# Kernel tuning notes

Measured on AMD Instinct MI355X. Metric: run time of the kernel, lower is better.

## Reference

```python
import jax, jax.numpy as jnp
import numpy as np

POOL = 7
IMG = 1024.0
NUM_CLASSES = 2
R = 1000


def crop_and_resize(feat, boxes, pool):
    # feat: [C,H,W]; boxes: [N,4] normalized (y1,x1,y2,x2); returns [N,C,pool,pool]
    C, H, W = feat.shape
    y1, x1, y2, x2 = boxes[:, 0], boxes[:, 1], boxes[:, 2], boxes[:, 3]
    t = jnp.arange(pool, dtype=feat.dtype) / (pool - 1)
    ys = (y1[:, None] + (y2 - y1)[:, None] * t[None, :]) * (H - 1)  # [N,P]
    xs = (x1[:, None] + (x2 - x1)[:, None] * t[None, :]) * (W - 1)  # [N,P]
    vy = (ys >= 0) & (ys <= H - 1)
    vx = (xs >= 0) & (xs <= W - 1)
    yf = jnp.floor(ys)
    xf = jnp.floor(xs)
    wy = (ys - yf)[None, :, :, None]  # [1,N,P,1]
    wx = (xs - xf)[None, :, None, :]  # [1,N,1,P]
    y0 = jnp.clip(yf, 0, H - 1).astype(jnp.int32)
    y1i = jnp.clip(yf + 1, 0, H - 1).astype(jnp.int32)
    x0 = jnp.clip(xf, 0, W - 1).astype(jnp.int32)
    x1i = jnp.clip(xf + 1, 0, W - 1).astype(jnp.int32)

    def g(yi, xi):  # gather -> [C,N,P,P]
        return feat[:, yi[:, :, None], xi[:, None, :]]

    val = (g(y0, x0) * (1 - wy) * (1 - wx)
           + g(y0, x1i) * (1 - wy) * wx
           + g(y1i, x0) * wy * (1 - wx)
           + g(y1i, x1i) * wy * wx)
    mask = (vy[:, :, None] & vx[:, None, :])[None]  # extrapolation value 0
    return jnp.where(mask, val, 0.0).transpose(1, 0, 2, 3)


def roi_align(feats, rois_flat):
    # rois_flat: [N,4] in pixel coords (x1,y1,x2,y2)
    x1, y1, x2, y2 = rois_flat[:, 0], rois_flat[:, 1], rois_flat[:, 2], rois_flat[:, 3]
    lvl = jnp.log2(jnp.sqrt((y2 - y1) * (x2 - x1)) / 224.0)
    lvl = jnp.clip(jnp.round(lvl) + 4, 2, 5)
    boxes = rois_flat[:, jnp.array([1, 0, 3, 2])] / IMG  # (y1,x1,y2,x2) normalized
    crops = jnp.stack([crop_and_resize(f[0], boxes, POOL) for f in feats])  # [4,N,C,P,P]
    sel = (lvl[None, :] == jnp.arange(2, 6, dtype=lvl.dtype)[:, None])       # [4,N]
    return jnp.sum(jnp.where(sel[:, :, None, None, None], crops, 0.0), axis=0)  # [N,C,P,P]


def setup_inputs() -> dict:
    key = jax.random.key(0)
    ks = jax.random.split(key, 24)
    feat2 = jax.random.normal(ks[0], (1, 256, 256, 256), jnp.float32)
    feat3 = jax.random.normal(ks[1], (1, 256, 128, 128), jnp.float32)
    feat4 = jax.random.normal(ks[2], (1, 256, 64, 64), jnp.float32)
    feat5 = jax.random.normal(ks[3], (1, 256, 32, 32), jnp.float32)
    x1 = jax.random.uniform(ks[4], (1, R), minval=0.0, maxval=900.0)
    y1 = jax.random.uniform(ks[5], (1, R), minval=0.0, maxval=900.0)
    w = jax.random.uniform(ks[6], (1, R), minval=16.0, maxval=400.0)
    h = jax.random.uniform(ks[7], (1, R), minval=16.0, maxval=400.0)
    rois = jnp.stack([x1, y1, jnp.minimum(x1 + w, 1023.0), jnp.minimum(y1 + h, 1023.0)], axis=-1)
    s = 0.02
    params = dict(
        conv_w=s * jax.random.normal(ks[8], (1024, 256, POOL, POOL), jnp.float32),
        conv_b=jnp.zeros((1024,), jnp.float32),
        bn_gamma=jnp.ones((1024,), jnp.float32),
        bn_beta=jnp.zeros((1024,), jnp.float32),
        bn_mean=jnp.zeros((1024,), jnp.float32),
        bn_var=jnp.ones((1024,), jnp.float32),
        fc1_w=s * jax.random.normal(ks[9], (1024, 1024), jnp.float32),
        fc1_b=jnp.zeros((1024,), jnp.float32),
        fc2_w=s * jax.random.normal(ks[10], (1024, 1024), jnp.float32),
        fc2_b=jnp.zeros((1024,), jnp.float32),
        cls_w=s * jax.random.normal(ks[11], (NUM_CLASSES, 1024), jnp.float32),
        cls_b=jnp.zeros((NUM_CLASSES,), jnp.float32),
        bbox_w=s * jax.random.normal(ks[12], (NUM_CLASSES * 4, 1024), jnp.float32),
        bbox_b=jnp.zeros((NUM_CLASSES * 4,), jnp.float32),
    )
    return dict(feat2=feat2, feat3=feat3, feat4=feat4, feat5=feat5, rois=rois, **params)


def reference(feat2, feat3, feat4, feat5, rois, conv_w, conv_b, bn_gamma, bn_beta,
              bn_mean, bn_var, fc1_w, fc1_b, fc2_w, fc2_b, cls_w, cls_b, bbox_w, bbox_b):
    roi_number = rois.shape[1]
    pooled = roi_align([feat2, feat3, feat4, feat5], rois.reshape(-1, 4))  # [N,256,7,7]
    # conv1 (7x7 valid on 7x7 input -> 1x1 spatial) + BN (inference stats, eps=1e-3)
    y = jnp.einsum('nchw,ochw->no', pooled, conv_w) + conv_b
    y = (y - bn_mean) / jnp.sqrt(bn_var + 1e-3) * bn_gamma + bn_beta
    h = jax.nn.relu(y @ fc1_w.T + fc1_b)
    h = jax.nn.relu(h @ fc2_w.T + fc2_b)
    logits = h @ cls_w.T + cls_b
    probs = jax.nn.softmax(logits, axis=-1)
    bbox = h @ bbox_w.T + bbox_b
    return (logits.reshape(1, roi_number, NUM_CLASSES),
            probs.reshape(1, roi_number, NUM_CLASSES),
            bbox.reshape(1, roi_number, NUM_CLASSES, 4))
```

## Files before the change

kernel.cpp:

```cpp
#include <hip/hip_runtime.h>
#include <cstdint>
#include <cstddef>

typedef __attribute__((ext_vector_type(8))) short bf16x8;
typedef __attribute__((ext_vector_type(4))) float f32x4;

#define POOLK 12544

#define TOFF2 0
#define TOFF3 16777216
#define TOFF4 20971520
#define TOFF5 22020096

__device__ __forceinline__ void gld16(const void* g, void* l) {
    __builtin_amdgcn_global_load_lds(
        (const __attribute__((address_space(1))) void*)g,
        (__attribute__((address_space(3))) void*)l, 16, 0, 0);
}
__device__ __forceinline__ unsigned short f32_to_bf16(float f) {
    union { float f; unsigned u; } x; x.f = f;
    return (unsigned short)((x.u + 0x7FFFu + ((x.u >> 16) & 1u)) >> 16);
}
__device__ __forceinline__ float bf16_to_f32(unsigned short s) {
    return __uint_as_float(((unsigned)s) << 16);
}

__global__ __launch_bounds__(256) void feat_tr_kernel(
    const float* __restrict__ f2, const float* __restrict__ f3,
    const float* __restrict__ f4, const float* __restrict__ f5,
    unsigned short* __restrict__ T)
{
    __shared__ __align__(16) unsigned short sh[128 * 256];
    int b = blockIdx.x;
    const float* src; unsigned short* dst; int P;
    if (b < 512)      { src = f2; dst = T + TOFF2; P = 65536; }
    else if (b < 640) { src = f3; dst = T + TOFF3; P = 16384; b -= 512; }
    else if (b < 672) { src = f4; dst = T + TOFF4; P = 4096;  b -= 640; }
    else              { src = f5; dst = T + TOFF5; P = 1024;  b -= 672; }
    const int p0 = b * 128;
    const int t = threadIdx.x;
    const int lane5 = t & 31;
    const int x4 = lane5 * 4;
    const int fx = (lane5 & 7) << 3;

#pragma unroll
    for (int it = 0; it < 8; ++it) {
        float4 v[4];
        int cs[4];
#pragma unroll
        for (int u = 0; u < 4; ++u) {
            cs[u] = it * 32 + u * 8 + (t >> 5);
            v[u] = *(const float4*)(src + (size_t)cs[u] * P + p0 + x4);
        }
#pragma unroll
        for (int u = 0; u < 4; ++u) {
            const int cp = cs[u] ^ fx;
            float vv[4] = {v[u].x, v[u].y, v[u].z, v[u].w};
#pragma unroll
            for (int i = 0; i < 4; ++i)
                sh[(x4 + i) * 256 + cp] = f32_to_bf16(vv[i]);
        }
    }
    __syncthreads();

    const int c0 = lane5 * 8;
#pragma unroll
    for (int oz = 0; oz < 16; ++oz) {
        const int pp = oz * 8 + (t >> 5);
        const int cr = c0 ^ (((pp >> 2) & 7) << 3);
        const bf16x8 vv = *(const bf16x8*)&sh[pp * 256 + cr];
        *(bf16x8*)(dst + (size_t)(p0 + pp) * 256 + c0) = vv;
    }
}

__global__ __launch_bounds__(256) void gather_prep_kernel(
    const unsigned short* __restrict__ T, const float* __restrict__ rois,
    unsigned short* __restrict__ pooled, int nroi,
    const float* __restrict__ conv_w, unsigned short* __restrict__ convw_bf,
    const float* __restrict__ fc1_w, unsigned short* __restrict__ fc1w_bf,
    const float* __restrict__ fc2_w, unsigned short* __restrict__ fc2w_bf)
{
    const int t = threadIdx.x;
    int b = blockIdx.x;

    if (b >= 1024) {
        b -= 1024;
        if (b < 2048) {
            __shared__ unsigned short sh[6272];
            const int o = b >> 1, half = b & 1;
            const float* srow = conv_w + (size_t)o * POOLK + half * 6272;
            for (int k = t; k < 6272; k += 256) sh[k] = f32_to_bf16(srow[k]);
            __syncthreads();
            unsigned short* drow = convw_bf + (size_t)o * POOLK + half * 128;
            for (int k = t; k < 6272; k += 256) {
                const int ij = k >> 7, cl = k & 127;
                drow[ij * 256 + cl] = sh[cl * 49 + ij];
            }
        } else {
            b -= 2048;
            const float* src = (b < 256) ? fc1_w : fc2_w;
            unsigned short* dst = (b < 256) ? fc1w_bf : fc2w_bf;
            const int base = (b & 255) * 4096 + t * 16;
#pragma unroll
            for (int u = 0; u < 4; ++u) {
                const float4 v = *(const float4*)(src + base + u * 4);
                ushort4 o4;
                o4.x = f32_to_bf16(v.x); o4.y = f32_to_bf16(v.y);
                o4.z = f32_to_bf16(v.z); o4.w = f32_to_bf16(v.w);
                *(ushort4*)(dst + base + u * 4) = o4;
            }
        }
        return;
    }

    const int n = b;
    unsigned short* orow = pooled + (size_t)n * POOLK;
    if (n >= nroi) {
        const bf16x8 z = {};
        for (int k = t * 8; k < POOLK; k += 2048) *(bf16x8*)(orow + k) = z;
        return;
    }
    __shared__ int sy0[7], sy1[7], sx0[7], sx1[7];
    __shared__ float swy[7], swx[7], svy[7], svx[7];

    const float rx1 = rois[n*4+0], ry1 = rois[n*4+1];
    const float rx2 = rois[n*4+2], ry2 = rois[n*4+3];
    int lvl = (int)rintf(log2f(sqrtf((ry2-ry1)*(rx2-rx1)) * (1.0f/224.0f))) + 4;
    lvl = lvl < 2 ? 2 : (lvl > 5 ? 5 : lvl);
    const int W = 256 >> (lvl - 2);
    const float Hm1 = (float)(W - 1);
    const unsigned short* Tl = T + (lvl == 2 ? TOFF2 : (lvl == 3 ? TOFF3 : (lvl == 4 ? TOFF4 : TOFF5)));

    if (t < 7) {
        const float tt = (float)t / 6.0f;
        const float by1 = ry1*(1.0f/1024.0f), by2 = ry2*(1.0f/1024.0f);
        const float bx1 = rx1*(1.0f/1024.0f), bx2 = rx2*(1.0f/1024.0f);
        const float ys = (by1 + (by2 - by1) * tt) * Hm1;
        const float xs = (bx1 + (bx2 - bx1) * tt) * Hm1;
        const float yf = floorf(ys), xf = floorf(xs);
        swy[t] = ys - yf;  swx[t] = xs - xf;
        sy0[t] = (int)fminf(fmaxf(yf,        0.0f), Hm1);
        sy1[t] = (int)fminf(fmaxf(yf + 1.0f, 0.0f), Hm1);
        sx0[t] = (int)fminf(fmaxf(xf,        0.0f), Hm1);
        sx1[t] = (int)fminf(fmaxf(xf + 1.0f, 0.0f), Hm1);
        svy[t] = (ys >= 0.0f && ys <= Hm1) ? 1.0f : 0.0f;
        svx[t] = (xs >= 0.0f && xs <= Hm1) ? 1.0f : 0.0f;
    }
    __syncthreads();

    const int g  = t >> 5;
    const int c0 = (t & 31) * 8;
#pragma unroll
    for (int it = 0; it < 7; ++it) {
        const int pos = it * 8 + g;
        if (pos >= 49) break;
        const int i = pos / 7, j = pos % 7;
        const int y0 = sy0[i], y1 = sy1[i], x0 = sx0[j], x1 = sx1[j];
        const float wy = swy[i], wx = swx[j];
        const float scale = svy[i] * svx[j];
        const bf16x8 v00 = *(const bf16x8*)(Tl + ((size_t)(y0*W + x0))*256 + c0);
        const bf16x8 v01 = *(const bf16x8*)(Tl + ((size_t)(y0*W + x1))*256 + c0);
        const bf16x8 v10 = *(const bf16x8*)(Tl + ((size_t)(y1*W + x0))*256 + c0);
        const bf16x8 v11 = *(const bf16x8*)(Tl + ((size_t)(y1*W + x1))*256 + c0);
        bf16x8 o;
#pragma unroll
        for (int jj = 0; jj < 8; ++jj) {
            const float f00 = bf16_to_f32((unsigned short)v00[jj]);
            const float f01 = bf16_to_f32((unsigned short)v01[jj]);
            const float f10 = bf16_to_f32((unsigned short)v10[jj]);
            const float f11 = bf16_to_f32((unsigned short)v11[jj]);
            const float top = f00 + (f01 - f00) * wx;
            const float bot = f10 + (f11 - f10) * wx;
            o[jj] = (short)f32_to_bf16((top + (bot - top) * wy) * scale);
        }
        *(bf16x8*)(orow + pos * 256 + c0) = o;
    }
}

__global__ __launch_bounds__(256) void roi_direct_kernel(
    const float* __restrict__ feat2, const float* __restrict__ feat3,
    const float* __restrict__ feat4, const float* __restrict__ feat5,
    const float* __restrict__ rois, unsigned short* __restrict__ pooled, int nroi)
{
    const int n = blockIdx.x;
    const int tid = threadIdx.x;
    unsigned short* orow = pooled + (size_t)n * POOLK;
    if (n >= nroi) {
        const bf16x8 z = {};
        for (int k = tid * 8; k < POOLK; k += 2048) *(bf16x8*)(orow + k) = z;
        return;
    }
    __shared__ int sy0[7], sy1[7], sx0[7], sx1[7];
    __shared__ float swy[7], swx[7], svy[7], svx[7];
    const float rx1 = rois[n*4+0], ry1 = rois[n*4+1];
    const float rx2 = rois[n*4+2], ry2 = rois[n*4+3];
    int lvl = (int)rintf(log2f(sqrtf((ry2-ry1)*(rx2-rx1)) * (1.0f/224.0f))) + 4;
    lvl = lvl < 2 ? 2 : (lvl > 5 ? 5 : lvl);
    const int H = 256 >> (lvl - 2);
    const float Hm1 = (float)(H - 1);
    const float* feat = lvl==2 ? feat2 : (lvl==3 ? feat3 : (lvl==4 ? feat4 : feat5));
    if (tid < 7) {
        const float t = (float)tid / 6.0f;
        const float by1 = ry1*(1.0f/1024.0f), by2 = ry2*(1.0f/1024.0f);
        const float bx1 = rx1*(1.0f/1024.0f), bx2 = rx2*(1.0f/1024.0f);
        const float ys = (by1 + (by2-by1)*t) * Hm1;
        const float xs = (bx1 + (bx2-bx1)*t) * Hm1;
        const float yf = floorf(ys), xf = floorf(xs);
        swy[tid] = ys - yf;  swx[tid] = xs - xf;
        sy0[tid] = (int)fminf(fmaxf(yf,      0.0f), Hm1);
        sy1[tid] = (int)fminf(fmaxf(yf+1.0f, 0.0f), Hm1);
        sx0[tid] = (int)fminf(fmaxf(xf,      0.0f), Hm1);
        sx1[tid] = (int)fminf(fmaxf(xf+1.0f, 0.0f), Hm1);
        svy[tid] = (ys >= 0.0f && ys <= Hm1) ? 1.0f : 0.0f;
        svx[tid] = (xs >= 0.0f && xs <= Hm1) ? 1.0f : 0.0f;
    }
    __syncthreads();
    const int HW = H * H;
    for (int e = tid; e < POOLK; e += 256) {
        const int c = e / 49, ij = e % 49, i = ij / 7, j = ij % 7;
        const float* p = feat + c * HW;
        const int y0 = sy0[i], y1 = sy1[i], x0 = sx0[j], x1 = sx1[j];
        const float wy = swy[i], wx = swx[j];
        const float v00 = p[y0*H + x0], v01 = p[y0*H + x1];
        const float v10 = p[y1*H + x0], v11 = p[y1*H + x1];
        float v = v00*(1.0f-wy)*(1.0f-wx) + v01*(1.0f-wy)*wx
                + v10*wy*(1.0f-wx)        + v11*wy*wx;
        v *= svy[i] * svx[j];
        orow[ij*256 + c] = f32_to_bf16(v);
    }
}

__global__ __launch_bounds__(256) void wprep_kernel(
    const float* __restrict__ conv_w, unsigned short* __restrict__ convw_bf,
    const float* __restrict__ fc1_w, unsigned short* __restrict__ fc1w_bf,
    const float* __restrict__ fc2_w, unsigned short* __restrict__ fc2w_bf)
{
    const int t = threadIdx.x;
    int b = blockIdx.x;
    if (b < 2048) {
        __shared__ unsigned short sh[6272];
        const int o = b >> 1, half = b & 1;
        const float* srow = conv_w + (size_t)o * POOLK + half * 6272;
        for (int k = t; k < 6272; k += 256) sh[k] = f32_to_bf16(srow[k]);
        __syncthreads();
        unsigned short* drow = convw_bf + (size_t)o * POOLK + half * 128;
        for (int k = t; k < 6272; k += 256) {
            const int ij = k >> 7, cl = k & 127;
            drow[ij * 256 + cl] = sh[cl * 49 + ij];
        }
        return;
    }
    b -= 2048;
    const float* src = (b < 256) ? fc1_w : fc2_w;
    unsigned short* dst = (b < 256) ? fc1w_bf : fc2w_bf;
    const int base = (b & 255) * 4096 + t * 16;
#pragma unroll
    for (int u = 0; u < 4; ++u) {
        const float4 v = *(const float4*)(src + base + u * 4);
        ushort4 o4;
        o4.x = f32_to_bf16(v.x); o4.y = f32_to_bf16(v.y);
        o4.z = f32_to_bf16(v.z); o4.w = f32_to_bf16(v.w);
        *(ushort4*)(dst + base + u * 4) = o4;
    }
}

__global__ __launch_bounds__(256, 2) void gemm_bt(
    const unsigned short* __restrict__ A, const unsigned short* __restrict__ B,
    float* __restrict__ Cpart, int K, int Kper, int nz)
{
    __shared__ __align__(16) unsigned short At[2][128*64];
    __shared__ __align__(16) unsigned short Bt[2][128*64];
    const int tid  = threadIdx.x;
    const int lane = tid & 63;
    const int bid  = blockIdx.x;
    const int z  = bid % nz;
    const int iq = bid / nz;
    const int bx = iq & 7, by = iq >> 3;
    const int wm = (tid >> 6) >> 1, wn = (tid >> 6) & 1;
    const size_t k0 = (size_t)z * Kper;

    const int r1 = tid >> 3;
    const int q  = tid & 7;
    const int csw = (q ^ (r1 & 7)) * 8;
    const unsigned short* Ag = A + ((size_t)(by * 128 + r1)) * K + k0 + csw;
    const unsigned short* Bg = B + ((size_t)(bx * 128 + r1)) * K + k0 + csw;
    const int nit = (Kper + 63) >> 6;

#pragma unroll
    for (int p = 0; p < 4; ++p) {
        gld16(Ag + (size_t)(32 * p) * K, &At[0][p * 2048 + tid * 8]);
        gld16(Bg + (size_t)(32 * p) * K, &Bt[0][p * 2048 + tid * 8]);
    }

    f32x4 acc[4][4] = {};
    const int fr = lane & 15;
    const int fq = lane >> 4;
    const int sA = fr & 7;

    int buf = 0;
    for (int it = 0; it < nit; ++it) {
        const int k = it << 6;
        if (it + 1 < nit) {
            const size_t ko = (size_t)(k + 64);
#pragma unroll
            for (int p = 0; p < 4; ++p) {
                gld16(Ag + (size_t)(32 * p) * K + ko, &At[buf ^ 1][p * 2048 + tid * 8]);
                gld16(Bg + (size_t)(32 * p) * K + ko, &Bt[buf ^ 1][p * 2048 + tid * 8]);
            }
            asm volatile("s_waitcnt vmcnt(8)" ::: "memory");
        } else {
            asm volatile("s_waitcnt vmcnt(0)" ::: "memory");
        }
        __builtin_amdgcn_sched_barrier(0);
        __builtin_amdgcn_s_barrier();
        __builtin_amdgcn_sched_barrier(0);

        bf16x8 a[4][2], b[4][2];
#pragma unroll
        for (int mi = 0; mi < 4; ++mi) {
            const int row = wm * 64 + mi * 16 + fr;
#pragma unroll
            for (int kk = 0; kk < 2; ++kk)
                a[mi][kk] = *(const bf16x8*)&At[buf][row * 64 + ((kk * 4 + fq) ^ sA) * 8];
        }
#pragma unroll
        for (int ni = 0; ni < 4; ++ni) {
            const int row = wn * 64 + ni * 16 + fr;
#pragma unroll
            for (int kk = 0; kk < 2; ++kk)
                b[ni][kk] = *(const bf16x8*)&Bt[buf][row * 64 + ((kk * 4 + fq) ^ sA) * 8];
        }
        __builtin_amdgcn_s_setprio(1);
#pragma unroll
        for (int mi = 0; mi < 4; ++mi)
#pragma unroll
            for (int ni = 0; ni < 4; ++ni)
                acc[mi][ni] = __builtin_amdgcn_mfma_f32_16x16x32_bf16(
                    a[mi][0], b[ni][0], acc[mi][ni], 0, 0, 0);
        if (k + 32 < Kper) {
#pragma unroll
            for (int mi = 0; mi < 4; ++mi)
#pragma unroll
                for (int ni = 0; ni < 4; ++ni)
                    acc[mi][ni] = __builtin_amdgcn_mfma_f32_16x16x32_bf16(
                        a[mi][1], b[ni][1], acc[mi][ni], 0, 0, 0);
        }
        __builtin_amdgcn_s_setprio(0);
        __builtin_amdgcn_sched_barrier(0);
        __builtin_amdgcn_s_barrier();
        __builtin_amdgcn_sched_barrier(0);
        buf ^= 1;
    }

    float* Cp = Cpart + (size_t)z * (1024 * 1024);
    const int row0 = by * 128 + wm * 64;
    const int col0 = bx * 128 + wn * 64;
#pragma unroll
    for (int mi = 0; mi < 4; ++mi)
#pragma unroll
        for (int ni = 0; ni < 4; ++ni)
#pragma unroll
            for (int r = 0; r < 4; ++r)
                Cp[(size_t)(row0 + mi*16 + fq*4 + r) * 1024 + col0 + ni*16 + fr]
                    = acc[mi][ni][r];
}

__global__ void reduce_bn_kernel(const float* __restrict__ part,
    const float* __restrict__ bias, const float* __restrict__ gamma,
    const float* __restrict__ beta, const float* __restrict__ mean,
    const float* __restrict__ var, unsigned short* __restrict__ out, int nz)
{
    const int i4 = (blockIdx.x * 256 + threadIdx.x) * 4;
    const int n = i4 & 1023;
    float4 v = make_float4(0.f, 0.f, 0.f, 0.f);
    for (int zz = 0; zz < nz; ++zz) {
        const float4 p = *(const float4*)(part + (size_t)zz * 1048576 + i4);
        v.x += p.x; v.y += p.y; v.z += p.z; v.w += p.w;
    }
    const float4 bi = *(const float4*)(bias + n);
    const float4 ga = *(const float4*)(gamma + n);
    const float4 be = *(const float4*)(beta + n);
    const float4 me = *(const float4*)(mean + n);
    const float4 va = *(const float4*)(var + n);
    ushort4 o;
    o.x = f32_to_bf16((v.x + bi.x - me.x) * __frsqrt_rn(va.x + 0.001f) * ga.x + be.x);
    o.y = f32_to_bf16((v.y + bi.y - me.y) * __frsqrt_rn(va.y + 0.001f) * ga.y + be.y);
    o.z = f32_to_bf16((v.z + bi.z - me.z) * __frsqrt_rn(va.z + 0.001f) * ga.z + be.z);
    o.w = f32_to_bf16((v.w + bi.w - me.w) * __frsqrt_rn(va.w + 0.001f) * ga.w + be.w);
    *(ushort4*)(out + i4) = o;
}

__global__ __launch_bounds__(256) void gemm64_fused(
    const unsigned short* __restrict__ A, const unsigned short* __restrict__ B,
    const float* __restrict__ bias, unsigned short* __restrict__ out, int relu)
{
    __shared__ __align__(16) unsigned short At[2][64*64];
    __shared__ __align__(16) unsigned short Bt[2][64*64];
    const int tid = threadIdx.x, lane = tid & 63;
    const int w = tid >> 6, wm = w >> 1, wn = w & 1;
    const int r1 = tid >> 3;
    const int q  = tid & 7;
    const int csw = (q ^ (r1 & 7)) * 8;
    const unsigned short* Ag = A + (size_t)(blockIdx.y*64 + r1) * 1024 + csw;
    const unsigned short* Bg = B + (size_t)(blockIdx.x*64 + r1) * 1024 + csw;
    const int fr = lane & 15, fq = lane >> 4;
    const int sA = fr & 7;

#pragma unroll
    for (int p = 0; p < 2; ++p) {
        gld16(Ag + (size_t)(32 * p) * 1024, &At[0][p * 2048 + tid * 8]);
        gld16(Bg + (size_t)(32 * p) * 1024, &Bt[0][p * 2048 + tid * 8]);
    }

    f32x4 acc[2][2] = {};
    int buf = 0;
    for (int it = 0; it < 16; ++it) {
        if (it + 1 < 16) {
            const int ko = (it + 1) * 64;
#pragma unroll
            for (int p = 0; p < 2; ++p) {
                gld16(Ag + (size_t)(32 * p) * 1024 + ko, &At[buf ^ 1][p * 2048 + tid * 8]);
                gld16(Bg + (size_t)(32 * p) * 1024 + ko, &Bt[buf ^ 1][p * 2048 + tid * 8]);
            }
            asm volatile("s_waitcnt vmcnt(4)" ::: "memory");
        } else {
            asm volatile("s_waitcnt vmcnt(0)" ::: "memory");
        }
        __builtin_amdgcn_sched_barrier(0);
        __builtin_amdgcn_s_barrier();
        __builtin_amdgcn_sched_barrier(0);

        bf16x8 a[2][2], b[2][2];
#pragma unroll
        for (int mi = 0; mi < 2; ++mi) {
            const int row = wm * 32 + mi * 16 + fr;
#pragma unroll
            for (int kk = 0; kk < 2; ++kk)
                a[mi][kk] = *(const bf16x8*)&At[buf][row * 64 + ((kk * 4 + fq) ^ sA) * 8];
        }
#pragma unroll
        for (int ni = 0; ni < 2; ++ni) {
            const int row = wn * 32 + ni * 16 + fr;
#pragma unroll
            for (int kk = 0; kk < 2; ++kk)
                b[ni][kk] = *(const bf16x8*)&Bt[buf][row * 64 + ((kk * 4 + fq) ^ sA) * 8];
        }
        __builtin_amdgcn_s_setprio(1);
#pragma unroll
        for (int kk = 0; kk < 2; ++kk)
#pragma unroll
            for (int mi = 0; mi < 2; ++mi)
#pragma unroll
                for (int ni = 0; ni < 2; ++ni)
                    acc[mi][ni] = __builtin_amdgcn_mfma_f32_16x16x32_bf16(
                        a[mi][kk], b[ni][kk], acc[mi][ni], 0, 0, 0);
        __builtin_amdgcn_s_setprio(0);
        __builtin_amdgcn_sched_barrier(0);
        __builtin_amdgcn_s_barrier();
        __builtin_amdgcn_sched_barrier(0);
        buf ^= 1;
    }
    const int row0 = blockIdx.y*64 + wm*32;
    const int col0 = blockIdx.x*64 + wn*32;
#pragma unroll
    for (int mi = 0; mi < 2; ++mi)
#pragma unroll
        for (int ni = 0; ni < 2; ++ni)
#pragma unroll
            for (int r = 0; r < 4; ++r) {
                const int row = row0 + mi*16 + fq*4 + r;
                const int col = col0 + ni*16 + fr;
                float v = acc[mi][ni][r] + bias[col];
                if (relu) v = fmaxf(v, 0.0f);
                out[(size_t)row * 1024 + col] = f32_to_bf16(v);
            }
}

__global__ __launch_bounds__(256) void head_kernel(
    const unsigned short* __restrict__ h2,
    const float* __restrict__ cls_w, const float* __restrict__ cls_b,
    const float* __restrict__ bbox_w, const float* __restrict__ bbox_b,
    float* __restrict__ out)
{
    const int roi = blockIdx.x * 4 + (threadIdx.x >> 6);
    const int lane = threadIdx.x & 63;
    const unsigned short* hrow = h2 + (size_t)roi * 1024;
    float hv[16];
#pragma unroll
    for (int j = 0; j < 16; ++j)
        hv[j] = bf16_to_f32(hrow[lane*16 + j]);
    float r[10];
#pragma unroll
    for (int o = 0; o < 10; ++o) {
        const float* w = (o < 2) ? (cls_w + o*1024) : (bbox_w + (size_t)(o-2)*1024);
        float s = 0.f;
#pragma unroll
        for (int j = 0; j < 16; ++j) s += hv[j] * w[lane*16 + j];
#pragma unroll
        for (int off = 32; off > 0; off >>= 1) s += __shfl_xor(s, off);
        r[o] = s;
    }
    if (lane == 0) {
        const float l0 = r[0] + cls_b[0], l1 = r[1] + cls_b[1];
        out[roi*2+0] = l0; out[roi*2+1] = l1;
        const float m = fmaxf(l0, l1);
        const float e0 = expf(l0 - m), e1 = expf(l1 - m);
        const float inv = 1.0f / (e0 + e1);
        out[2000 + roi*2 + 0] = e0 * inv;
        out[2000 + roi*2 + 1] = e1 * inv;
#pragma unroll
        for (int qq = 0; qq < 8; ++qq) out[4000 + roi*8 + qq] = r[2+qq] + bbox_b[qq];
    }
}

extern "C" void kernel_launch(void* const* d_in, const int* in_sizes, int n_in,
                              void* d_out, int out_size, void* d_ws, size_t ws_size,
                              hipStream_t stream)
{
    const float* feat2   = (const float*)d_in[0];
    const float* feat3   = (const float*)d_in[1];
    const float* feat4   = (const float*)d_in[2];
    const float* feat5   = (const float*)d_in[3];
    const float* rois    = (const float*)d_in[4];
    const float* conv_w  = (const float*)d_in[5];
    const float* conv_b  = (const float*)d_in[6];
    const float* bn_gamma= (const float*)d_in[7];
    const float* bn_beta = (const float*)d_in[8];
    const float* bn_mean = (const float*)d_in[9];
    const float* bn_var  = (const float*)d_in[10];
    const float* fc1_w   = (const float*)d_in[11];
    const float* fc1_b   = (const float*)d_in[12];
    const float* fc2_w   = (const float*)d_in[13];
    const float* fc2_b   = (const float*)d_in[14];
    const float* cls_w   = (const float*)d_in[15];
    const float* cls_b   = (const float*)d_in[16];
    const float* bbox_w  = (const float*)d_in[17];
    const float* bbox_b  = (const float*)d_in[18];
    float* out = (float*)d_out;
    const int nroi = in_sizes[4] / 4;

    const size_t fixedBytes = (size_t)25690112 + 25690112 + 5 * (size_t)2097152;
    const size_t needA = fixedBytes + (size_t)44564480;
    const int tier = (ws_size >= needA) ? 1 : 2;
    const size_t regionA = tier == 1 ? (size_t)44564480 : (size_t)16777216;
    const int nzc  = tier == 1 ? 8 : 4;
    const int Kper = tier == 1 ? 1568 : 3136;

    char* ws = (char*)d_ws;
    size_t off = 0;
    auto alloc = [&](size_t bytes) {
        void* p = ws + off; off += (bytes + 255) & ~(size_t)255; return p;
    };
    char* rA = (char*)alloc(regionA);
    unsigned short* T    = (unsigned short*)rA;
    float*          part = (float*)rA;
    unsigned short* pooled   = (unsigned short*)alloc((size_t)1024 * POOLK * 2);
    unsigned short* convw_bf = (unsigned short*)alloc((size_t)1024 * POOLK * 2);
    unsigned short* fc1w_bf  = (unsigned short*)alloc((size_t)1048576 * 2);
    unsigned short* fc2w_bf  = (unsigned short*)alloc((size_t)1048576 * 2);
    unsigned short* ybf      = (unsigned short*)alloc((size_t)1048576 * 2);
    unsigned short* h1bf     = (unsigned short*)alloc((size_t)1048576 * 2);
    unsigned short* h2bf     = (unsigned short*)alloc((size_t)1048576 * 2);

    if (tier == 1) {
        hipLaunchKernelGGL(feat_tr_kernel, dim3(680), dim3(256), 0, stream,
                           feat2, feat3, feat4, feat5, T);
        hipLaunchKernelGGL(gather_prep_kernel, dim3(3584), dim3(256), 0, stream,
                           T, rois, pooled, nroi,
                           conv_w, convw_bf, fc1_w, fc1w_bf, fc2_w, fc2w_bf);
    } else {
        hipLaunchKernelGGL(wprep_kernel, dim3(2560), dim3(256), 0, stream,
                           conv_w, convw_bf, fc1_w, fc1w_bf, fc2_w, fc2w_bf);
        hipLaunchKernelGGL(roi_direct_kernel, dim3(1024), dim3(256), 0, stream,
                           feat2, feat3, feat4, feat5, rois, pooled, nroi);
    }

    hipLaunchKernelGGL(gemm_bt, dim3(64 * nzc), dim3(256), 0, stream,
                       pooled, convw_bf, part, POOLK, Kper, nzc);
    hipLaunchKernelGGL(reduce_bn_kernel, dim3(1024), dim3(256), 0, stream,
                       part, conv_b, bn_gamma, bn_beta, bn_mean, bn_var, ybf, nzc);

    hipLaunchKernelGGL(gemm64_fused, dim3(16, 16), dim3(256), 0, stream,
                       ybf, fc1w_bf, fc1_b, h1bf, 1);
    hipLaunchKernelGGL(gemm64_fused, dim3(16, 16), dim3(256), 0, stream,
                       h1bf, fc2w_bf, fc2_b, h2bf, 1);

    hipLaunchKernelGGL(head_kernel, dim3(250), dim3(256), 0, stream,
                       h2bf, cls_w, cls_b, bbox_w, bbox_b, out);
}
```

Measured before the change: 125.1 us.

## Retile conv GEMM to 128x64 tiles with 32-wide K steps

The split-K conv GEMM moves from 128x128 tiles with a 64-element K step to 128x64 tiles with a 32-element K step, so twice as many blocks launch. Shared memory per block shrinks, the occupancy hint rises from 2 to 3 blocks per CU, and a new XOR swizzle with interleaved row placement is used for the LDS layout. The goal is more parallelism and better latency hiding. The cost is less operand reuse per tile, which means more global and LDS traffic per FLOP, and more barriers per unit of work.

```diff
diff --git a/kernel.cpp b/kernel.cpp
--- a/kernel.cpp
+++ b/kernel.cpp
@@ -264,50 +264,44 @@
     }
 }
 
-__global__ __launch_bounds__(256, 2) void gemm_bt(
+__global__ __launch_bounds__(256, 3) void gemm_bt(
     const unsigned short* __restrict__ A, const unsigned short* __restrict__ B,
     float* __restrict__ Cpart, int K, int Kper, int nz)
 {
-    __shared__ __align__(16) unsigned short At[2][128*64];
-    __shared__ __align__(16) unsigned short Bt[2][128*64];
+    __shared__ __align__(16) unsigned short At[2][4096];
+    __shared__ __align__(16) unsigned short Bt[2][2048];
     const int tid  = threadIdx.x;
     const int lane = tid & 63;
     const int bid  = blockIdx.x;
     const int z  = bid % nz;
     const int iq = bid / nz;
-    const int bx = iq & 7, by = iq >> 3;
-    const int wm = (tid >> 6) >> 1, wn = (tid >> 6) & 1;
+    const int bx = iq & 15, by = iq >> 4;
+    const int wid = tid >> 6;
+    const int wm = wid >> 1, wn = wid & 1;
     const size_t k0 = (size_t)z * Kper;
 
-    const int r1 = tid >> 3;
-    const int q  = tid & 7;
-    const int csw = (q ^ (r1 & 7)) * 8;
-    const unsigned short* Ag = A + ((size_t)(by * 128 + r1)) * K + k0 + csw;
-    const unsigned short* Bg = B + ((size_t)(bx * 128 + r1)) * K + k0 + csw;
-    const int nit = (Kper + 63) >> 6;
-
-#pragma unroll
-    for (int p = 0; p < 4; ++p) {
-        gld16(Ag + (size_t)(32 * p) * K, &At[0][p * 2048 + tid * 8]);
-        gld16(Bg + (size_t)(32 * p) * K, &Bt[0][p * 2048 + tid * 8]);
-    }
-
-    f32x4 acc[4][4] = {};
+    const int mloc = ((tid >> 3) << 1) | ((tid >> 2) & 1);
+    const int kq   = (tid & 3) ^ ((tid >> 3) & 3);
+    const unsigned short* Ag = A + ((size_t)(by * 128 + mloc)) * K + k0 + kq * 8;
+    const unsigned short* Bg = B + ((size_t)(bx * 64 + mloc)) * K + k0 + kq * 8;
+    const int nit = Kper >> 5;
+
+    gld16(Ag,                  &At[0][tid * 8]);
+    gld16(Ag + (size_t)64 * K, &At[0][2048 + tid * 8]);
+    gld16(Bg,                  &Bt[0][tid * 8]);
+
+    f32x4 acc[4][2] = {};
     const int fr = lane & 15;
     const int fq = lane >> 4;
-    const int sA = fr & 7;
 
     int buf = 0;
     for (int it = 0; it < nit; ++it) {
-        const int k = it << 6;
         if (it + 1 < nit) {
-            const size_t ko = (size_t)(k + 64);
-#pragma unroll
-            for (int p = 0; p < 4; ++p) {
-                gld16(Ag + (size_t)(32 * p) * K + ko, &At[buf ^ 1][p * 2048 + tid * 8]);
-                gld16(Bg + (size_t)(32 * p) * K + ko, &Bt[buf ^ 1][p * 2048 + tid * 8]);
-            }
-            asm volatile("s_waitcnt vmcnt(8)" ::: "memory");
+            const size_t ko = (size_t)(it + 1) * 32;
+            gld16(Ag + ko,                  &At[buf ^ 1][tid * 8]);
+            gld16(Ag + (size_t)64 * K + ko, &At[buf ^ 1][2048 + tid * 8]);
+            gld16(Bg + ko,                  &Bt[buf ^ 1][tid * 8]);
+            asm volatile("s_waitcnt vmcnt(3)" ::: "memory");
         } else {
             asm volatile("s_waitcnt vmcnt(0)" ::: "memory");
         }
@@ -315,36 +309,26 @@
         __builtin_amdgcn_s_barrier();
         __builtin_amdgcn_sched_barrier(0);
 
-        bf16x8 a[4][2], b[4][2];
+        bf16x8 a[4], b[2];
 #pragma unroll
         for (int mi = 0; mi < 4; ++mi) {
-            const int row = wm * 64 + mi * 16 + fr;
-#pragma unroll
-            for (int kk = 0; kk < 2; ++kk)
-                a[mi][kk] = *(const bf16x8*)&At[buf][row * 64 + ((kk * 4 + fq) ^ sA) * 8];
-        }
-#pragma unroll
-        for (int ni = 0; ni < 4; ++ni) {
-            const int row = wn * 64 + ni * 16 + fr;
-#pragma unroll
-            for (int kk = 0; kk < 2; ++kk)
-                b[ni][kk] = *(const bf16x8*)&Bt[buf][row * 64 + ((kk * 4 + fq) ^ sA) * 8];
+            const int m = wm * 64 + mi * 16 + fr;
+            a[mi] = *(const bf16x8*)&At[buf][((m >> 1) << 6) + ((m & 1) << 5)
+                                            + ((fq ^ ((m >> 1) & 3)) << 3)];
+        }
+#pragma unroll
+        for (int ni = 0; ni < 2; ++ni) {
+            const int m = wn * 32 + ni * 16 + fr;
+            b[ni] = *(const bf16x8*)&Bt[buf][((m >> 1) << 6) + ((m & 1) << 5)
+                                            + ((fq ^ ((m >> 1) & 3)) << 3)];
         }
         __builtin_amdgcn_s_setprio(1);
 #pragma unroll
         for (int mi = 0; mi < 4; ++mi)
 #pragma unroll
-            for (int ni = 0; ni < 4; ++ni)
+            for (int ni = 0; ni < 2; ++ni)
                 acc[mi][ni] = __builtin_amdgcn_mfma_f32_16x16x32_bf16(
-                    a[mi][0], b[ni][0], acc[mi][ni], 0, 0, 0);
-        if (k + 32 < Kper) {
-#pragma unroll
-            for (int mi = 0; mi < 4; ++mi)
-#pragma unroll
-                for (int ni = 0; ni < 4; ++ni)
-                    acc[mi][ni] = __builtin_amdgcn_mfma_f32_16x16x32_bf16(
-                        a[mi][1], b[ni][1], acc[mi][ni], 0, 0, 0);
-        }
+                    a[mi], b[ni], acc[mi][ni], 0, 0, 0);
         __builtin_amdgcn_s_setprio(0);
         __builtin_amdgcn_sched_barrier(0);
         __builtin_amdgcn_s_barrier();
@@ -354,11 +338,11 @@
 
     float* Cp = Cpart + (size_t)z * (1024 * 1024);
     const int row0 = by * 128 + wm * 64;
-    const int col0 = bx * 128 + wn * 64;
+    const int col0 = bx * 64 + wn * 32;
 #pragma unroll
     for (int mi = 0; mi < 4; ++mi)
 #pragma unroll
-        for (int ni = 0; ni < 4; ++ni)
+        for (int ni = 0; ni < 2; ++ni)
 #pragma unroll
             for (int r = 0; r < 4; ++r)
                 Cp[(size_t)(row0 + mi*16 + fq*4 + r) * 1024 + col0 + ni*16 + fr]
@@ -575,7 +559,7 @@
                            feat2, feat3, feat4, feat5, rois, pooled, nroi);
     }
 
-    hipLaunchKernelGGL(gemm_bt, dim3(64 * nzc), dim3(256), 0, stream,
+    hipLaunchKernelGGL(gemm_bt, dim3(128 * nzc), dim3(256), 0, stream,
                        pooled, convw_bf, part, POOLK, Kper, nzc);
     hipLaunchKernelGGL(reduce_bn_kernel, dim3(1024), dim3(256), 0, stream,
                        part, conv_b, bn_gamma, bn_beta, bn_mean, bn_var, ybf, nzc);
```

Result: slower. 130.5 us (+4.3%).

## Fuse split-K reduction and BN into GEMM via last-block counter; vectorize conv weight prep

Applied to the files above, without the earlier changes.

The conv GEMM now ends with an atomic per-tile counter. The last split-K block for each output tile sums the partials, applies bias and batch norm, and writes bf16, so the separate reduce kernel launch is gone. A memset of the counters is added. Separately, the conv weight transpose-and-convert processes a full row per block with float4 loads and 16-byte stores instead of half rows with scalar stores. The trade-offs are a serial tail on the last block per tile, the threadfence and atomic cost, and a 25KB LDS footprint for the prep blocks.

```diff
diff --git a/kernel.cpp b/kernel.cpp
--- a/kernel.cpp
+++ b/kernel.cpp
@@ -85,19 +85,28 @@
 
     if (b >= 1024) {
         b -= 1024;
-        if (b < 2048) {
-            __shared__ unsigned short sh[6272];
-            const int o = b >> 1, half = b & 1;
-            const float* srow = conv_w + (size_t)o * POOLK + half * 6272;
-            for (int k = t; k < 6272; k += 256) sh[k] = f32_to_bf16(srow[k]);
+        if (b < 1024) {
+            __shared__ __align__(16) unsigned short shw[POOLK];
+            const float* srow = conv_w + (size_t)b * POOLK;
+            for (int k4 = t; k4 < 3136; k4 += 256) {
+                const float4 v = *(const float4*)(srow + k4 * 4);
+                ushort4 o4;
+                o4.x = f32_to_bf16(v.x); o4.y = f32_to_bf16(v.y);
+                o4.z = f32_to_bf16(v.z); o4.w = f32_to_bf16(v.w);
+                *(ushort4*)(&shw[k4 * 4]) = o4;
+            }
             __syncthreads();
-            unsigned short* drow = convw_bf + (size_t)o * POOLK + half * 128;
-            for (int k = t; k < 6272; k += 256) {
-                const int ij = k >> 7, cl = k & 127;
-                drow[ij * 256 + cl] = sh[cl * 49 + ij];
+            unsigned short* drow = convw_bf + (size_t)b * POOLK;
+            for (int e = t; e < 1568; e += 256) {
+                const int p = e * 8;
+                const int ij = p >> 8, c0 = p & 255;
+                bf16x8 o8;
+#pragma unroll
+                for (int c = 0; c < 8; ++c) o8[c] = (short)shw[(c0 + c) * 49 + ij];
+                *(bf16x8*)(drow + p) = o8;
             }
         } else {
-            b -= 2048;
+            b -= 1024;
             const float* src = (b < 256) ? fc1_w : fc2_w;
             unsigned short* dst = (b < 256) ? fc1w_bf : fc2w_bf;
             const int base = (b & 255) * 4096 + t * 16;
@@ -237,20 +246,29 @@
 {
     const int t = threadIdx.x;
     int b = blockIdx.x;
-    if (b < 2048) {
-        __shared__ unsigned short sh[6272];
-        const int o = b >> 1, half = b & 1;
-        const float* srow = conv_w + (size_t)o * POOLK + half * 6272;
-        for (int k = t; k < 6272; k += 256) sh[k] = f32_to_bf16(srow[k]);
+    if (b < 1024) {
+        __shared__ __align__(16) unsigned short shw[POOLK];
+        const float* srow = conv_w + (size_t)b * POOLK;
+        for (int k4 = t; k4 < 3136; k4 += 256) {
+            const float4 v = *(const float4*)(srow + k4 * 4);
+            ushort4 o4;
+            o4.x = f32_to_bf16(v.x); o4.y = f32_to_bf16(v.y);
+            o4.z = f32_to_bf16(v.z); o4.w = f32_to_bf16(v.w);
+            *(ushort4*)(&shw[k4 * 4]) = o4;
+        }
         __syncthreads();
-        unsigned short* drow = convw_bf + (size_t)o * POOLK + half * 128;
-        for (int k = t; k < 6272; k += 256) {
-            const int ij = k >> 7, cl = k & 127;
-            drow[ij * 256 + cl] = sh[cl * 49 + ij];
+        unsigned short* drow = convw_bf + (size_t)b * POOLK;
+        for (int e = t; e < 1568; e += 256) {
+            const int p = e * 8;
+            const int ij = p >> 8, c0 = p & 255;
+            bf16x8 o8;
+#pragma unroll
+            for (int c = 0; c < 8; ++c) o8[c] = (short)shw[(c0 + c) * 49 + ij];
+            *(bf16x8*)(drow + p) = o8;
         }
         return;
     }
-    b -= 2048;
+    b -= 1024;
     const float* src = (b < 256) ? fc1_w : fc2_w;
     unsigned short* dst = (b < 256) ? fc1w_bf : fc2w_bf;
     const int base = (b & 255) * 4096 + t * 16;
@@ -266,10 +284,15 @@
 
 __global__ __launch_bounds__(256, 2) void gemm_bt(
     const unsigned short* __restrict__ A, const unsigned short* __restrict__ B,
-    float* __restrict__ Cpart, int K, int Kper, int nz)
+    float* __restrict__ Cpart,
+    const float* __restrict__ bias, const float* __restrict__ gamma,
+    const float* __restrict__ beta, const float* __restrict__ mean,
+    const float* __restrict__ var, unsigned short* __restrict__ outbf,
+    int* __restrict__ cnt, int K, int Kper, int nz)
 {
     __shared__ __align__(16) unsigned short At[2][128*64];
     __shared__ __align__(16) unsigned short Bt[2][128*64];
+    __shared__ int lastFlag;
     const int tid  = threadIdx.x;
     const int lane = tid & 63;
     const int bid  = blockIdx.x;
@@ -363,31 +386,39 @@
             for (int r = 0; r < 4; ++r)
                 Cp[(size_t)(row0 + mi*16 + fq*4 + r) * 1024 + col0 + ni*16 + fr]
                     = acc[mi][ni][r];
-}
-
-__global__ void reduce_bn_kernel(const float* __restrict__ part,
-    const float* __restrict__ bias, const float* __restrict__ gamma,
-    const float* __restrict__ beta, const float* __restrict__ mean,
-    const float* __restrict__ var, unsigned short* __restrict__ out, int nz)
-{
-    const int i4 = (blockIdx.x * 256 + threadIdx.x) * 4;
-    const int n = i4 & 1023;
-    float4 v = make_float4(0.f, 0.f, 0.f, 0.f);
-    for (int zz = 0; zz < nz; ++zz) {
-        const float4 p = *(const float4*)(part + (size_t)zz * 1048576 + i4);
-        v.x += p.x; v.y += p.y; v.z += p.z; v.w += p.w;
-    }
-    const float4 bi = *(const float4*)(bias + n);
-    const float4 ga = *(const float4*)(gamma + n);
-    const float4 be = *(const float4*)(beta + n);
-    const float4 me = *(const float4*)(mean + n);
-    const float4 va = *(const float4*)(var + n);
-    ushort4 o;
-    o.x = f32_to_bf16((v.x + bi.x - me.x) * __frsqrt_rn(va.x + 0.001f) * ga.x + be.x);
-    o.y = f32_to_bf16((v.y + bi.y - me.y) * __frsqrt_rn(va.y + 0.001f) * ga.y + be.y);
-    o.z = f32_to_bf16((v.z + bi.z - me.z) * __frsqrt_rn(va.z + 0.001f) * ga.z + be.z);
-    o.w = f32_to_bf16((v.w + bi.w - me.w) * __frsqrt_rn(va.w + 0.001f) * ga.w + be.w);
-    *(ushort4*)(out + i4) = o;
+
+    __threadfence();
+    if (tid == 0) {
+        const int old = __hip_atomic_fetch_add(&cnt[iq], 1,
+                            __ATOMIC_ACQ_REL, __HIP_MEMORY_SCOPE_AGENT);
+        lastFlag = (old == nz - 1);
+    }
+    __syncthreads();
+    if (!lastFlag) return;
+
+    const int trow0 = by * 128, tcol0 = bx * 128;
+    for (int e = tid; e < 128 * 32; e += 256) {
+        const int r  = e >> 5;
+        const int c4 = (e & 31) * 4;
+        const size_t idx = (size_t)(trow0 + r) * 1024 + tcol0 + c4;
+        float4 v = make_float4(0.f, 0.f, 0.f, 0.f);
+        for (int zz = 0; zz < nz; ++zz) {
+            const float4 p = *(const float4*)(Cpart + (size_t)zz * 1048576 + idx);
+            v.x += p.x; v.y += p.y; v.z += p.z; v.w += p.w;
+        }
+        const int n = tcol0 + c4;
+        const float4 bi = *(const float4*)(bias + n);
+        const float4 ga = *(const float4*)(gamma + n);
+        const float4 be = *(const float4*)(beta + n);
+        const float4 me = *(const float4*)(mean + n);
+        const float4 va = *(const float4*)(var + n);
+        ushort4 o;
+        o.x = f32_to_bf16((v.x + bi.x - me.x) * __frsqrt_rn(va.x + 0.001f) * ga.x + be.x);
+        o.y = f32_to_bf16((v.y + bi.y - me.y) * __frsqrt_rn(va.y + 0.001f) * ga.y + be.y);
+        o.z = f32_to_bf16((v.z + bi.z - me.z) * __frsqrt_rn(va.z + 0.001f) * ga.z + be.z);
+        o.w = f32_to_bf16((v.w + bi.w - me.w) * __frsqrt_rn(va.w + 0.001f) * ga.w + be.w);
+        *(ushort4*)(outbf + idx) = o;
+    }
 }
 
 __global__ __launch_bounds__(256) void gemm64_fused(
@@ -539,7 +570,7 @@
     float* out = (float*)d_out;
     const int nroi = in_sizes[4] / 4;
 
-    const size_t fixedBytes = (size_t)25690112 + 25690112 + 5 * (size_t)2097152;
+    const size_t fixedBytes = (size_t)25690112 + 25690112 + 5 * (size_t)2097152 + 4096;
     const size_t needA = fixedBytes + (size_t)44564480;
     const int tier = (ws_size >= needA) ? 1 : 2;
     const size_t regionA = tier == 1 ? (size_t)44564480 : (size_t)16777216;
@@ -561,24 +592,27 @@
     unsigned short* ybf      = (unsigned short*)alloc((size_t)1048576 * 2);
     unsigned short* h1bf     = (unsigned short*)alloc((size_t)1048576 * 2);
     unsigned short* h2bf     = (unsigned short*)alloc((size_t)1048576 * 2);
+    int*            cnt      = (int*)alloc(256);
+
+    hipMemsetAsync(cnt, 0, 256, stream);
 
     if (tier == 1) {
         hipLaunchKernelGGL(feat_tr_kernel, dim3(680), dim3(256), 0, stream,
                            feat2, feat3, feat4, feat5, T);
-        hipLaunchKernelGGL(gather_prep_kernel, dim3(3584), dim3(256), 0, stream,
+        hipLaunchKernelGGL(gather_prep_kernel, dim3(2560), dim3(256), 0, stream,
                            T, rois, pooled, nroi,
                            conv_w, convw_bf, fc1_w, fc1w_bf, fc2_w, fc2w_bf);
     } else {
-        hipLaunchKernelGGL(wprep_kernel, dim3(2560), dim3(256), 0, stream,
+        hipLaunchKernelGGL(wprep_kernel, dim3(1536), dim3(256), 0, stream,
                            conv_w, convw_bf, fc1_w, fc1w_bf, fc2_w, fc2w_bf);
         hipLaunchKernelGGL(roi_direct_kernel, dim3(1024), dim3(256), 0, stream,
                            feat2, feat3, feat4, feat5, rois, pooled, nroi);
     }
 
     hipLaunchKernelGGL(gemm_bt, dim3(64 * nzc), dim3(256), 0, stream,
-                       pooled, convw_bf, part, POOLK, Kper, nzc);
-    hipLaunchKernelGGL(reduce_bn_kernel, dim3(1024), dim3(256), 0, stream,
-                       part, conv_b, bn_gamma, bn_beta, bn_mean, bn_var, ybf, nzc);
+                       pooled, convw_bf, part,
+                       conv_b, bn_gamma, bn_beta, bn_mean, bn_var, ybf,
+                       cnt, POOLK, Kper, nzc);
 
     hipLaunchKernelGGL(gemm64_fused, dim3(16, 16), dim3(256), 0, stream,
                        ybf, fc1w_bf, fc1_b, h1bf, 1);
```

Measured after the change: 240.2 us. 1.92x slower.
